# Performance work log

Measured on AMD Instinct MI355X. Metric: run time of the kernel, lower is better.

The kernel has to match this reference:

```python
import jax, jax.numpy as jnp
import numpy as np

HEADS = 8
DIM_HEAD = 32
SCALE = DIM_HEAD ** -0.5


def _split_heads(t):
    # [b, n, h*d] -> [b, h, n, d]
    b, n, hd = t.shape
    return t.reshape(b, n, HEADS, hd // HEADS).transpose(0, 2, 1, 3)


def setup_inputs() -> dict:
    key = jax.random.key(0)
    k1, k2, k3, k4 = jax.random.split(key, 4)
    b, n, dim = 2, 2048, 256
    inner = HEADS * DIM_HEAD  # 256
    x = jax.random.normal(k1, (b, n, dim), dtype=jnp.float32)
    attn_feat = jax.random.normal(k2, (b, n, dim), dtype=jnp.float32)
    # nn.Linear(dim, 3*inner, bias=False): store as [dim, 3*inner] for x @ W
    W_qkv = jax.random.normal(k3, (dim, 3 * inner), dtype=jnp.float32) * (dim ** -0.5)
    W_qkv_aux = jax.random.normal(k4, (dim, 3 * inner), dtype=jnp.float32) * (dim ** -0.5)
    return {"x": x, "attn_feat": attn_feat, "W_qkv": W_qkv, "W_qkv_aux": W_qkv_aux,
            "use_cls_tokens": 1}


def reference(x, attn_feat, W_qkv, W_qkv_aux, use_cls_tokens):
    b, n, dim = x.shape
    # aux Q,K (v_aux computed but unused, matching original chunk of 3)
    qkv_aux = attn_feat @ W_qkv_aux            # [b, n, 3*inner]
    q_aux, k_aux, _ = jnp.split(qkv_aux, 3, axis=-1)
    q_aux, k_aux = _split_heads(q_aux), _split_heads(k_aux)
    # self Q,K
    qkv_self = x @ W_qkv
    q_self, k_self, _ = jnp.split(qkv_self, 3, axis=-1)
    q_self, k_self = _split_heads(q_self), _split_heads(k_self)
    # dual score product: (QK^T_aux * scale) * (QK^T_self * scale)
    dots_aux = jnp.einsum('bhid,bhjd->bhij', q_aux, k_aux) * SCALE
    dots_self = jnp.einsum('bhid,bhjd->bhij', q_self, k_self) * SCALE
    attn = jax.nn.softmax(dots_aux * dots_self, axis=-1)  # [b, h, n, n]
    # v = x.unsqueeze(1): broadcast raw x over heads
    out = jnp.einsum('bhij,bjd->bhid', attn, x)           # [b, h, n, dim]
    out = out.transpose(0, 2, 1, 3).reshape(b, n, HEADS * dim)
    attn_flat = attn.transpose(0, 2, 1, 3).reshape(b, n, HEADS * n)
    return (out, out[:, 0], attn_flat[:, 0])
```

## Files before the change

kernel.cpp:

```cpp
#include <hip/hip_runtime.h>

typedef _Float16 f16;
typedef _Float16 f16x4 __attribute__((ext_vector_type(4)));
typedef _Float16 f16x8 __attribute__((ext_vector_type(8)));
typedef float f32x4 __attribute__((ext_vector_type(4)));

#define LOG2E 1.4426950408889634f
#define SCL   (1.4426950408889634f / 32.0f)
#define TH_RAW 177.445f

__global__ __launch_bounds__(256) void k_W(const float* __restrict__ Wq,
    const float* __restrict__ Wa, f16* __restrict__ Wt) {
  __shared__ f16 tile[64][65];
  int n0 = blockIdx.x * 64, k0 = blockIdx.y * 64, s = blockIdx.z;
  const float* W = s ? Wa : Wq;
  f16* dst = Wt + (size_t)s * 512 * 256;
  int t = threadIdx.x, c = t & 63, rg = t >> 6;
#pragma unroll
  for (int r = 0; r < 16; ++r) {
    int krow = r * 4 + rg;
    tile[krow][c] = (f16)W[(size_t)(k0 + krow) * 768 + n0 + c];
  }
  __syncthreads();
#pragma unroll
  for (int r = 0; r < 16; ++r) {
    int nrow = r * 4 + rg;
    dst[(size_t)(n0 + nrow) * 256 + k0 + c] = tile[c][nrow];
  }
}

__global__ __launch_bounds__(256) void k_proj(const float* __restrict__ x,
    const float* __restrict__ af, const f16* __restrict__ Wt,
    f16* __restrict__ Qs, f16* __restrict__ Ks,
    f16* __restrict__ Qa, f16* __restrict__ Ka, f16* __restrict__ xt) {
  __shared__ f16 tile[64][65];
  int t = threadIdx.x;
  if (blockIdx.x >= 64) {
    int r = ((blockIdx.z * 8 + blockIdx.y) * 16 + (blockIdx.x - 64));
    int n0 = (r & 31) * 64, d0 = ((r >> 5) & 3) * 64, b = r >> 7;
    int c = t & 63, rg = t >> 6;
#pragma unroll
    for (int rr = 0; rr < 16; ++rr) {
      int row = rr * 4 + rg;
      tile[row][c] = (f16)x[((size_t)b * 2048 + n0 + row) * 256 + d0 + c];
    }
    __syncthreads();
#pragma unroll
    for (int rr = 0; rr < 16; ++rr) {
      int drow = rr * 4 + rg;
      xt[((size_t)b * 256 + d0 + drow) * 2048 + n0 + c] = tile[c][drow];
    }
    return;
  }
  int mt = blockIdx.x, nt = blockIdx.y, s = blockIdx.z;
  const float* A = s ? af : x;
  const f16* W = Wt + (size_t)s * 512 * 256;
  f16* Qd = s ? Qa : Qs;
  f16* Kd = s ? Ka : Ks;
  int wv = t >> 6, ln = t & 63, cl = ln & 15, g = ln >> 4;
  int m0 = mt * 64, n0 = nt * 64;
  const float* arow = A + (size_t)(m0 + wv * 16 + cl) * 256 + g * 8;
  const f16* wb = W + (size_t)n0 * 256 + g * 8;
  f32x4 z4 = {0.f, 0.f, 0.f, 0.f};
  f32x4 acc[4] = {z4, z4, z4, z4};
#pragma unroll
  for (int k32 = 0; k32 < 8; ++k32) {
    float4 u = *(const float4*)(arow + k32 * 32);
    float4 v = *(const float4*)(arow + k32 * 32 + 4);
    f16x8 a = { (f16)u.x, (f16)u.y, (f16)u.z, (f16)u.w,
                (f16)v.x, (f16)v.y, (f16)v.z, (f16)v.w };
#pragma unroll
    for (int n4 = 0; n4 < 4; ++n4) {
      f16x8 bf = *(const f16x8*)(wb + (size_t)(n4 * 16 + cl) * 256 + k32 * 32);
      acc[n4] = __builtin_amdgcn_mfma_f32_16x16x32_f16(a, bf, acc[n4], 0, 0, 0);
    }
  }
#pragma unroll
  for (int n4 = 0; n4 < 4; ++n4) {
    int c = n0 + n4 * 16 + cl;
    int head = (c & 255) >> 5, d = c & 31;
    f16* dst = (c < 256) ? Qd : Kd;
#pragma unroll
    for (int r = 0; r < 4; ++r) {
      int m = m0 + wv * 16 + g * 4 + r;
      int bb = m >> 11, nn = m & 2047;
      dst[(((size_t)bb * 8 + head) * 2048 + nn) * 32 + d] = (f16)acc[n4][r];
    }
  }
}

__global__ __launch_bounds__(256, 2) void k_flash(const f16* __restrict__ Qs,
    const f16* __restrict__ Ks, const f16* __restrict__ Qa,
    const f16* __restrict__ Ka, const f16* __restrict__ xt,
    float* __restrict__ out, float* __restrict__ out_cls,
    float* __restrict__ attn0) {
  __shared__ f16 KaL[2][64][40];
  __shared__ f16 KsL[2][64][40];
  __shared__ f16 PL[2][64][72];
  __shared__ float alphaL[2][64] __attribute__((aligned(16)));
  __shared__ int   rsF[2][4] __attribute__((aligned(16)));
  __shared__ float lL[64];
  int h = blockIdx.y, b = blockIdx.z;
  int bh = b * 8 + h;
  int t = threadIdx.x;

  if (blockIdx.x == 0) {
    int wv = t >> 6;
    f16x8 qa8[4], qs8[4];
#pragma unroll
    for (int c = 0; c < 4; ++c) {
      qa8[c] = *(const f16x8*)&Qa[(size_t)bh * 2048 * 32 + c * 8];
      qs8[c] = *(const f16x8*)&Qs[(size_t)bh * 2048 * 32 + c * 8];
    }
    float sv[8];
#pragma unroll
    for (int r = 0; r < 8; ++r) {
      int j = r * 256 + t;
      const f16x8* ka8 = (const f16x8*)&Ka[((size_t)bh * 2048 + j) * 32];
      const f16x8* ks8 = (const f16x8*)&Ks[((size_t)bh * 2048 + j) * 32];
      float da = 0.f, ds = 0.f;
#pragma unroll
      for (int c = 0; c < 4; ++c) {
        f16x8 va = ka8[c], vs = ks8[c];
#pragma unroll
        for (int d = 0; d < 8; ++d) {
          da += (float)qa8[c][d] * (float)va[d];
          ds += (float)qs8[c][d] * (float)vs[d];
        }
      }
      sv[r] = da * ds * (1.f / 32.f);
    }
    float mx = sv[0];
#pragma unroll
    for (int r = 1; r < 8; ++r) mx = fmaxf(mx, sv[r]);
#pragma unroll
    for (int off = 1; off < 64; off <<= 1)
      mx = fmaxf(mx, __shfl_xor(mx, off, 64));
    if ((t & 63) == 0) lL[wv] = mx;
    __syncthreads();
    float m = fmaxf(fmaxf(lL[0], lL[1]), fmaxf(lL[2], lL[3]));
    float e[8], sum = 0.f;
#pragma unroll
    for (int r = 0; r < 8; ++r) {
      e[r] = exp2f((sv[r] - m) * LOG2E);
      sum += e[r];
    }
#pragma unroll
    for (int off = 1; off < 64; off <<= 1)
      sum += __shfl_xor(sum, off, 64);
    if ((t & 63) == 0) lL[4 + wv] = sum;
    __syncthreads();
    float l = (lL[4] + lL[5]) + (lL[6] + lL[7]);
#pragma unroll
    for (int r = 0; r < 8; ++r)
      attn0[(size_t)b * 16384 + h * 2048 + r * 256 + t] = e[r] / l;
    return;
  }

  int qt = blockIdx.x - 1;
  int wv = t >> 6, ln = t & 63, cl = ln & 15, g = ln >> 4;
  int qrow0 = qt * 64 + wv * 16;
  f16x8 qsf = *(const f16x8*)&Qs[((size_t)bh * 2048 + qrow0 + cl) * 32 + g * 8];
  f16x8 qaf = *(const f16x8*)&Qa[((size_t)bh * 2048 + qrow0 + cl) * 32 + g * 8];
  f32x4 z4 = {0.f, 0.f, 0.f, 0.f};
  f32x4 acc[4][4];
#pragma unroll
  for (int i = 0; i < 4; ++i)
#pragma unroll
    for (int j = 0; j < 4; ++j) acc[i][j] = z4;
  float m_run = -3.0e38f, l_lane = 0.f;
  int krow = t >> 2, koff = (t & 3) * 8;
  const f16* kaSrc = Ka + ((size_t)bh * 2048 + krow) * 32 + koff;
  const f16* ksSrc = Ks + ((size_t)bh * 2048 + krow) * 32 + koff;
  const f16* xb = xt + ((size_t)b * 256 + wv * 64) * 2048;

  float tv[16];
  f16x8 xf[2][4];

  auto SCORE_MM = [&](int buf) {
#pragma unroll
    for (int jt = 0; jt < 4; ++jt) {
      f16x8 kaf = *(const f16x8*)&KaL[buf][jt * 16 + cl][g * 8];
      f16x8 ksf = *(const f16x8*)&KsL[buf][jt * 16 + cl][g * 8];
      f32x4 za = __builtin_amdgcn_mfma_f32_16x16x32_f16(kaf, qaf, z4, 0, 0, 0);
      f32x4 zs = __builtin_amdgcn_mfma_f32_16x16x32_f16(ksf, qsf, z4, 0, 0, 0);
#pragma unroll
      for (int r = 0; r < 4; ++r) tv[jt * 4 + r] = za[r] * zs[r];
    }
  };

  auto SCORE_FIN = [&](int buf) {
    float a0 = fmaxf(tv[0], tv[1]),   a1 = fmaxf(tv[2], tv[3]);
    float a2 = fmaxf(tv[4], tv[5]),   a3 = fmaxf(tv[6], tv[7]);
    float a4 = fmaxf(tv[8], tv[9]),   a5 = fmaxf(tv[10], tv[11]);
    float a6 = fmaxf(tv[12], tv[13]), a7 = fmaxf(tv[14], tv[15]);
    float b0 = fmaxf(a0, a1), b1 = fmaxf(a2, a3);
    float b2 = fmaxf(a4, a5), b3 = fmaxf(a6, a7);
    float lmax = fmaxf(fmaxf(b0, b1), fmaxf(b2, b3));
    int wflag = 0;
    if (__any(lmax > m_run + TH_RAW)) {
      float tm = fmaxf(lmax, __shfl_xor(lmax, 16, 64));
      tm = fmaxf(tm, __shfl_xor(tm, 32, 64));
      float m_new = fmaxf(m_run, tm);
      float alpha = exp2f((m_run - m_new) * SCL);
      l_lane *= alpha;
      m_run = m_new;
      if (g == 0) alphaL[buf][wv * 16 + cl] = alpha;
      wflag = 1;
    }
    float mS = m_run * SCL;
    float p[16];
#pragma unroll
    for (int i = 0; i < 16; ++i) p[i] = exp2f(fmaf(tv[i], SCL, -mS));
    float s0 = p[0] + p[1],   s1 = p[2] + p[3];
    float s2 = p[4] + p[5],   s3 = p[6] + p[7];
    float s4 = p[8] + p[9],   s5 = p[10] + p[11];
    float s6 = p[12] + p[13], s7 = p[14] + p[15];
    float u0 = s0 + s1, u1 = s2 + s3, u2 = s4 + s5, u3 = s6 + s7;
    l_lane += (u0 + u1) + (u2 + u3);
#pragma unroll
    for (int jt = 0; jt < 4; ++jt) {
      auto lo = __builtin_amdgcn_cvt_pkrtz(p[jt * 4 + 0], p[jt * 4 + 1]);
      auto hi = __builtin_amdgcn_cvt_pkrtz(p[jt * 4 + 2], p[jt * 4 + 3]);
      f16x4 pk = { (f16)lo[0], (f16)lo[1], (f16)hi[0], (f16)hi[1] };
      *(f16x4*)&PL[buf][wv * 16 + cl][jt * 16 + g * 4] = pk;
    }
    if (ln == 0) rsF[buf][wv] = wflag;
  };

  auto XFLOAD = [&](int kt) {
#pragma unroll
    for (int ks2 = 0; ks2 < 2; ++ks2)
#pragma unroll
      for (int ddt = 0; ddt < 4; ++ddt)
        xf[ks2][ddt] = *(const f16x8*)(xb + (size_t)(ddt * 16 + cl) * 2048 +
                                       kt * 64 + ks2 * 32 + g * 8);
  };

  auto PVDO = [&](int pbuf) {
    int4 fl = *(const int4*)&rsF[pbuf][0];
    int flq[4] = { fl.x, fl.y, fl.z, fl.w };
#pragma unroll
    for (int qt2 = 0; qt2 < 4; ++qt2) {
      if (flq[qt2]) {
        f32x4 a4 = *(const f32x4*)&alphaL[pbuf][qt2 * 16 + g * 4];
#pragma unroll
        for (int ddt = 0; ddt < 4; ++ddt)
#pragma unroll
          for (int r = 0; r < 4; ++r) acc[qt2][ddt][r] *= a4[r];
      }
    }
#pragma unroll
    for (int ks2 = 0; ks2 < 2; ++ks2) {
      f16x8 pf[4];
#pragma unroll
      for (int qt2 = 0; qt2 < 4; ++qt2)
        pf[qt2] = *(const f16x8*)&PL[pbuf][qt2 * 16 + cl][ks2 * 32 + g * 8];
#pragma unroll
      for (int ddt = 0; ddt < 4; ++ddt)
#pragma unroll
        for (int qt2 = 0; qt2 < 4; ++qt2)
          acc[qt2][ddt] = __builtin_amdgcn_mfma_f32_16x16x32_f16(
              pf[qt2], xf[ks2][ddt], acc[qt2][ddt], 0, 0, 0);
    }
  };

  *(f16x8*)&KaL[0][krow][koff] = *(const f16x8*)kaSrc;
  *(f16x8*)&KsL[0][krow][koff] = *(const f16x8*)ksSrc;
  __syncthreads();

  f16x8 kan = *(const f16x8*)(kaSrc + 2048);
  f16x8 ksn = *(const f16x8*)(ksSrc + 2048);
  SCORE_MM(0);
  SCORE_FIN(0);
  *(f16x8*)&KaL[1][krow][koff] = kan;
  *(f16x8*)&KsL[1][krow][koff] = ksn;
  __syncthreads();

  for (int k = 1; k < 32; ++k) {
    int sbuf = k & 1, pbuf = sbuf ^ 1;
    XFLOAD(k - 1);
    if (k < 31) {
      kan = *(const f16x8*)(kaSrc + (size_t)(k + 1) * 2048);
      ksn = *(const f16x8*)(ksSrc + (size_t)(k + 1) * 2048);
    }
    SCORE_MM(sbuf);
    PVDO(pbuf);
    SCORE_FIN(sbuf);
    if (k < 31) {
      *(f16x8*)&KaL[pbuf][krow][koff] = kan;
      *(f16x8*)&KsL[pbuf][krow][koff] = ksn;
    }
    __syncthreads();
  }

  XFLOAD(31);
  PVDO(1);

  l_lane += __shfl_xor(l_lane, 16, 64);
  l_lane += __shfl_xor(l_lane, 32, 64);
  if (g == 0) lL[wv * 16 + cl] = l_lane;
  __syncthreads();
#pragma unroll
  for (int qt2 = 0; qt2 < 4; ++qt2) {
#pragma unroll
    for (int r = 0; r < 4; ++r) {
      float linv = 1.0f / lL[qt2 * 16 + g * 4 + r];
      int q = qt * 64 + qt2 * 16 + g * 4 + r;
#pragma unroll
      for (int ddt = 0; ddt < 4; ++ddt) {
        float v = acc[qt2][ddt][r] * linv;
        int col = h * 256 + wv * 64 + ddt * 16 + cl;
        out[((size_t)b * 2048 + q) * 2048 + col] = v;
        if (q == 0) out_cls[(size_t)b * 2048 + col] = v;
      }
    }
  }
}

extern "C" void kernel_launch(void* const* d_in, const int* in_sizes, int n_in,
                              void* d_out, int out_size, void* d_ws, size_t ws_size,
                              hipStream_t stream) {
  const float* x  = (const float*)d_in[0];
  const float* af = (const float*)d_in[1];
  const float* Wq = (const float*)d_in[2];
  const float* Wa = (const float*)d_in[3];
  const size_t QK = (size_t)2 * 8 * 2048 * 32;
  f16* Qs = (f16*)d_ws;
  f16* Ks = Qs + QK;
  f16* Qa = Ks + QK;
  f16* Ka = Qa + QK;
  f16* xt = Ka + QK;
  f16* Wt = xt + QK;
  float* out     = (float*)d_out;
  float* out_cls = out + (size_t)2 * 2048 * 2048;
  float* attn0   = out_cls + 2 * 2048;

  k_W<<<dim3(8, 4, 2), 256, 0, stream>>>(Wq, Wa, Wt);
  k_proj<<<dim3(80, 8, 2), 256, 0, stream>>>(x, af, Wt, Qs, Ks, Qa, Ka, xt);
  k_flash<<<dim3(33, 8, 2), 256, 0, stream>>>(Qs, Ks, Qa, Ka, xt, out, out_cls,
                                              attn0);
}
```

Measured before the change: 173.2 us.

## Fuse attention row-0 output into flash kernel via stored running-max history

```diff
diff --git a/kernel.cpp b/kernel.cpp
--- a/kernel.cpp
+++ b/kernel.cpp
@@ -100,65 +100,13 @@
   __shared__ float alphaL[2][64] __attribute__((aligned(16)));
   __shared__ int   rsF[2][4] __attribute__((aligned(16)));
   __shared__ float lL[64];
-  int h = blockIdx.y, b = blockIdx.z;
+  __shared__ float mHist[32];
+  __shared__ float mFinS;
+  int qt = blockIdx.x, h = blockIdx.y, b = blockIdx.z;
   int bh = b * 8 + h;
-  int t = threadIdx.x;
-
-  if (blockIdx.x == 0) {
-    int wv = t >> 6;
-    f16x8 qa8[4], qs8[4];
-#pragma unroll
-    for (int c = 0; c < 4; ++c) {
-      qa8[c] = *(const f16x8*)&Qa[(size_t)bh * 2048 * 32 + c * 8];
-      qs8[c] = *(const f16x8*)&Qs[(size_t)bh * 2048 * 32 + c * 8];
-    }
-    float sv[8];
-#pragma unroll
-    for (int r = 0; r < 8; ++r) {
-      int j = r * 256 + t;
-      const f16x8* ka8 = (const f16x8*)&Ka[((size_t)bh * 2048 + j) * 32];
-      const f16x8* ks8 = (const f16x8*)&Ks[((size_t)bh * 2048 + j) * 32];
-      float da = 0.f, ds = 0.f;
-#pragma unroll
-      for (int c = 0; c < 4; ++c) {
-        f16x8 va = ka8[c], vs = ks8[c];
-#pragma unroll
-        for (int d = 0; d < 8; ++d) {
-          da += (float)qa8[c][d] * (float)va[d];
-          ds += (float)qs8[c][d] * (float)vs[d];
-        }
-      }
-      sv[r] = da * ds * (1.f / 32.f);
-    }
-    float mx = sv[0];
-#pragma unroll
-    for (int r = 1; r < 8; ++r) mx = fmaxf(mx, sv[r]);
-#pragma unroll
-    for (int off = 1; off < 64; off <<= 1)
-      mx = fmaxf(mx, __shfl_xor(mx, off, 64));
-    if ((t & 63) == 0) lL[wv] = mx;
-    __syncthreads();
-    float m = fmaxf(fmaxf(lL[0], lL[1]), fmaxf(lL[2], lL[3]));
-    float e[8], sum = 0.f;
-#pragma unroll
-    for (int r = 0; r < 8; ++r) {
-      e[r] = exp2f((sv[r] - m) * LOG2E);
-      sum += e[r];
-    }
-#pragma unroll
-    for (int off = 1; off < 64; off <<= 1)
-      sum += __shfl_xor(sum, off, 64);
-    if ((t & 63) == 0) lL[4 + wv] = sum;
-    __syncthreads();
-    float l = (lL[4] + lL[5]) + (lL[6] + lL[7]);
-#pragma unroll
-    for (int r = 0; r < 8; ++r)
-      attn0[(size_t)b * 16384 + h * 2048 + r * 256 + t] = e[r] / l;
-    return;
-  }
-
-  int qt = blockIdx.x - 1;
-  int wv = t >> 6, ln = t & 63, cl = ln & 15, g = ln >> 4;
+  int t = threadIdx.x, wv = t >> 6, ln = t & 63, cl = ln & 15, g = ln >> 4;
+  bool isA0 = (qt == 0) && (wv == 0);
+  float* a0base = attn0 + (size_t)b * 16384 + h * 2048;
   int qrow0 = qt * 64 + wv * 16;
   f16x8 qsf = *(const f16x8*)&Qs[((size_t)bh * 2048 + qrow0 + cl) * 32 + g * 8];
   f16x8 qaf = *(const f16x8*)&Qa[((size_t)bh * 2048 + qrow0 + cl) * 32 + g * 8];
@@ -189,7 +137,7 @@
     }
   };
 
-  auto SCORE_FIN = [&](int buf) {
+  auto SCORE_FIN = [&](int buf, int kt) {
     float a0 = fmaxf(tv[0], tv[1]),   a1 = fmaxf(tv[2], tv[3]);
     float a2 = fmaxf(tv[4], tv[5]),   a3 = fmaxf(tv[6], tv[7]);
     float a4 = fmaxf(tv[8], tv[9]),   a5 = fmaxf(tv[10], tv[11]);
@@ -226,6 +174,17 @@
       *(f16x4*)&PL[buf][wv * 16 + cl][jt * 16 + g * 4] = pk;
     }
     if (ln == 0) rsF[buf][wv] = wflag;
+    if (isA0) {
+      if (ln == 0) mHist[kt] = m_run;
+      if (cl == 0) {
+#pragma unroll
+        for (int jt = 0; jt < 4; ++jt) {
+          float4 pw = { p[jt * 4 + 0], p[jt * 4 + 1],
+                        p[jt * 4 + 2], p[jt * 4 + 3] };
+          *(float4*)(a0base + kt * 64 + jt * 16 + g * 4) = pw;
+        }
+      }
+    }
   };
 
   auto XFLOAD = [&](int kt) {
@@ -272,7 +231,7 @@
   f16x8 kan = *(const f16x8*)(kaSrc + 2048);
   f16x8 ksn = *(const f16x8*)(ksSrc + 2048);
   SCORE_MM(0);
-  SCORE_FIN(0);
+  SCORE_FIN(0, 0);
   *(f16x8*)&KaL[1][krow][koff] = kan;
   *(f16x8*)&KsL[1][krow][koff] = ksn;
   __syncthreads();
@@ -286,7 +245,7 @@
     }
     SCORE_MM(sbuf);
     PVDO(pbuf);
-    SCORE_FIN(sbuf);
+    SCORE_FIN(sbuf, k);
     if (k < 31) {
       *(f16x8*)&KaL[pbuf][krow][koff] = kan;
       *(f16x8*)&KsL[pbuf][krow][koff] = ksn;
@@ -300,6 +259,7 @@
   l_lane += __shfl_xor(l_lane, 16, 64);
   l_lane += __shfl_xor(l_lane, 32, 64);
   if (g == 0) lL[wv * 16 + cl] = l_lane;
+  if (isA0 && ln == 0) mFinS = m_run;
   __syncthreads();
 #pragma unroll
   for (int qt2 = 0; qt2 < 4; ++qt2) {
@@ -314,6 +274,14 @@
         out[((size_t)b * 2048 + q) * 2048 + col] = v;
         if (q == 0) out_cls[(size_t)b * 2048 + col] = v;
       }
+    }
+  }
+  if (qt == 0) {
+    float l0inv = 1.0f / lL[0];
+    float mf = mFinS;
+    for (int i = t; i < 2048; i += 256) {
+      float v = a0base[i];
+      a0base[i] = v * exp2f((mHist[i >> 6] - mf) * SCL) * l0inv;
     }
   }
 }
@@ -338,6 +306,6 @@
 
   k_W<<<dim3(8, 4, 2), 256, 0, stream>>>(Wq, Wa, Wt);
   k_proj<<<dim3(80, 8, 2), 256, 0, stream>>>(x, af, Wt, Qs, Ks, Qa, Ka, xt);
-  k_flash<<<dim3(33, 8, 2), 256, 0, stream>>>(Qs, Ks, Qa, Ka, xt, out, out_cls,
+  k_flash<<<dim3(32, 8, 2), 256, 0, stream>>>(Qs, Ks, Qa, Ka, xt, out, out_cls,
                                               attn0);
 }
```

After: 174.5 us (median of 2 runs). No clear change (+0.8%).
